# Performance work log

Measured on AMD Instinct MI355X. Metric: run time of the kernel, lower is better.

Reference implementation:

```python
import jax, jax.numpy as jnp
import numpy as np

B, T, D = 2, 2048, 1024
N_HEADS = 16
HEAD_DIM = D // N_HEADS


def setup_inputs() -> dict:
    key = jax.random.key(0)
    ks = jax.random.split(key, 5)
    s = 0.02
    return {
        "x": jax.random.normal(ks[0], (B, T, D), jnp.float32),
        "wq": jax.random.normal(ks[1], (D, D), jnp.float32) * s,
        "wk": jax.random.normal(ks[2], (D, D), jnp.float32) * s,
        "wv": jax.random.normal(ks[3], (D, D), jnp.float32) * s,
        "wo": jax.random.normal(ks[4], (D, D), jnp.float32) * s,
        "bo": jnp.zeros((D,), jnp.float32),
    }


def reference(x, wq, wk, wv, wo, bo):
    b, t, _ = x.shape
    # QKV projections (weights stored [d_in, d_out]); reshape to (b, heads, t, head_dim)
    def split_heads(y):
        return y.reshape(b, t, N_HEADS, HEAD_DIM).transpose(0, 2, 1, 3)
    q = split_heads(x @ wq)
    k = split_heads(x @ wk)
    v = split_heads(x @ wv)
    # causal attention scores: (b, h, t, t)
    scores = jnp.einsum("bhqd,bhkd->bhqk", q, k)
    causal = jnp.tril(jnp.ones((t, t), bool))  # True where attending allowed
    scores = jnp.where(causal, scores, -jnp.inf)
    attn = jax.nn.softmax(scores / np.sqrt(HEAD_DIM).astype(np.float32), axis=-1)
    # dropout_rate = 0.0 (eval mode) -> identity
    ctx = jnp.einsum("bhqk,bhkd->bhqd", attn, v)
    ctx = ctx.transpose(0, 2, 1, 3).reshape(b, t, D)
    return ctx @ wo + bo
```

## Files before the change

kernel.cpp:

```cpp
#include <hip/hip_runtime.h>
#include <hip/hip_bf16.h>
#include <cstdint>

typedef __hip_bfloat16 bf16;
typedef __bf16 bf16x8 __attribute__((ext_vector_type(8)));
typedef __bf16 bf16x4 __attribute__((ext_vector_type(4)));
typedef float f32x4 __attribute__((ext_vector_type(4)));
typedef uint32_t u32x4 __attribute__((ext_vector_type(4)));

#define LOG2E 1.4426950408889634f

__device__ __forceinline__ void gload_lds16(const void* g, void* l) {
  __builtin_amdgcn_global_load_lds(
      (const __attribute__((address_space(1))) unsigned int*)g,
      (__attribute__((address_space(3))) unsigned int*)l,
      16, 0, 0);
}

__device__ __forceinline__ uint32_t pack_bf16(float a, float b) {
  const uint32_t ha = (uint32_t)__builtin_bit_cast(uint16_t, (__bf16)a);
  const uint32_t hb = (uint32_t)__builtin_bit_cast(uint16_t, (__bf16)b);
  return ha | (hb << 16);
}

__global__ void conv_k(const float* __restrict__ src, bf16* __restrict__ dst, int n) {
  const int i = (blockIdx.x * 256 + threadIdx.x) * 8;
  if (i >= n) return;
  const f32x4 a = *(const f32x4*)(src + i);
  const f32x4 b = *(const f32x4*)(src + i + 4);
  bf16x8 o;
#pragma unroll
  for (int j = 0; j < 4; ++j) { o[j] = (__bf16)a[j]; o[4 + j] = (__bf16)b[j]; }
  *(bf16x8*)(dst + i) = o;
}

__global__ void transpose_conv4(
    const float* __restrict__ wq, const float* __restrict__ wk,
    const float* __restrict__ wv, const float* __restrict__ wo,
    bf16* __restrict__ dqkv, bf16* __restrict__ dout) {
  __shared__ float tile[32][33];
  const int z = blockIdx.z;
  const float* src = (z == 0) ? wq : ((z == 1) ? wk : ((z == 2) ? wv : wo));
  bf16* dst = (z < 3) ? (dqkv + (long)z * 1048576) : dout;
  const int bx = blockIdx.x * 32, by = blockIdx.y * 32;
  const int tx = threadIdx.x;
  for (int j = threadIdx.y; j < 32; j += 8)
    tile[j][tx] = src[(long)(by + j) * 1024 + bx + tx];
  __syncthreads();
  for (int j = threadIdx.y; j < 32; j += 8)
    dst[(long)(bx + j) * 1024 + by + tx] = __float2bfloat16(tile[tx][j]);
}

__global__ __launch_bounds__(256, 2) void gemm_qkv(
    const bf16* __restrict__ A, const bf16* __restrict__ Bt,
    bf16* __restrict__ Cq, bf16* __restrict__ Ck, bf16* __restrict__ Cv,
    int M, int N, int K) {
  __shared__ __align__(16) bf16 As[128 * 32];
  __shared__ __align__(16) bf16 Bs[128 * 32];

  const int tid = threadIdx.x;
  const int lane = tid & 63;
  const int wave = tid >> 6;
  const int quad = lane >> 4;
  const int l16 = lane & 15;
  const int m0 = blockIdx.y * 128;
  const int n0 = blockIdx.x * 128;
  const int wm = (wave >> 1) * 64;
  const int wn = (wave & 1) * 64;

  const f32x4 zero4 = {0.f, 0.f, 0.f, 0.f};
  f32x4 acc[4][4];
#pragma unroll
  for (int mi = 0; mi < 4; ++mi)
#pragma unroll
    for (int ni = 0; ni < 4; ++ni) acc[mi][ni] = zero4;

  const int sRow = tid >> 2;
  const int sK = (tid & 3) * 8;
  const bf16* Ag = A + (long)(m0 + sRow) * K + sK;
  const bf16* Ag2 = Ag + 64L * K;
  const bf16* Bg = Bt + (long)(n0 + sRow) * K + sK;
  const bf16* Bg2 = Bg + 64L * K;

  for (int k0 = 0; k0 < K; k0 += 32) {
    gload_lds16(Ag + k0, &As[tid * 8]);
    gload_lds16(Ag2 + k0, &As[tid * 8 + 2048]);
    gload_lds16(Bg + k0, &Bs[tid * 8]);
    gload_lds16(Bg2 + k0, &Bs[tid * 8 + 2048]);
    __syncthreads();

    bf16x8 af[4], bfv[4];
#pragma unroll
    for (int mi = 0; mi < 4; ++mi)
      af[mi] = *(const bf16x8*)&As[(wm + mi * 16 + l16) * 32 + quad * 8];
#pragma unroll
    for (int ni = 0; ni < 4; ++ni)
      bfv[ni] = *(const bf16x8*)&Bs[(wn + ni * 16 + l16) * 32 + quad * 8];
#pragma unroll
    for (int mi = 0; mi < 4; ++mi)
#pragma unroll
      for (int ni = 0; ni < 4; ++ni)
        acc[mi][ni] = __builtin_amdgcn_mfma_f32_16x16x32_bf16(af[mi], bfv[ni], acc[mi][ni], 0, 0, 0);
    __syncthreads();
  }

#pragma unroll
  for (int mi = 0; mi < 4; ++mi) {
    const int gmb = m0 + wm + mi * 16 + quad * 4;
#pragma unroll
    for (int ni = 0; ni < 4; ++ni) {
      const int n = n0 + wn + ni * 16 + l16;
      const int which = n >> 10, rem = n & 1023;
      const int h = rem >> 6, hd = rem & 63;
      bf16* dst = (which == 0) ? Cq : ((which == 1) ? Ck : Cv);
#pragma unroll
      for (int r = 0; r < 4; ++r) {
        const int gm = gmb + r;
        const int b = gm >> 11, t = gm & 2047;
        dst[(((long)(b * 16 + h)) * 2048 + t) * 64 + hd] = __float2bfloat16(acc[mi][ni][r]);
      }
    }
  }
}

__global__ __launch_bounds__(256, 4) void gemm_out(
    const bf16* __restrict__ A, const bf16* __restrict__ Bt,
    const float* __restrict__ bias, float* __restrict__ Cout,
    int M, int N, int K) {
  __shared__ __align__(16) bf16 As[64 * 32];
  __shared__ __align__(16) bf16 Bs[128 * 32];

  const int tid = threadIdx.x;
  const int lane = tid & 63;
  const int wave = tid >> 6;
  const int quad = lane >> 4;
  const int l16 = lane & 15;
  const int m0 = blockIdx.y * 64;
  const int n0 = blockIdx.x * 128;
  const int wm = (wave & 1) * 32;
  const int wn = (wave >> 1) * 64;

  const f32x4 zero4 = {0.f, 0.f, 0.f, 0.f};
  f32x4 acc[2][4];
#pragma unroll
  for (int mi = 0; mi < 2; ++mi)
#pragma unroll
    for (int ni = 0; ni < 4; ++ni) acc[mi][ni] = zero4;

  const int sRow = tid >> 2;
  const int sK = (tid & 3) * 8;
  const bf16* Ag = A + (long)(m0 + sRow) * K + sK;
  const bf16* Bg = Bt + (long)(n0 + sRow) * K + sK;
  const bf16* Bg2 = Bg + 64L * K;

  for (int k0 = 0; k0 < K; k0 += 32) {
    gload_lds16(Ag + k0, &As[tid * 8]);
    gload_lds16(Bg + k0, &Bs[tid * 8]);
    gload_lds16(Bg2 + k0, &Bs[tid * 8 + 2048]);
    __syncthreads();

    bf16x8 af[2], bfv[4];
#pragma unroll
    for (int mi = 0; mi < 2; ++mi)
      af[mi] = *(const bf16x8*)&As[(wm + mi * 16 + l16) * 32 + quad * 8];
#pragma unroll
    for (int ni = 0; ni < 4; ++ni)
      bfv[ni] = *(const bf16x8*)&Bs[(wn + ni * 16 + l16) * 32 + quad * 8];
#pragma unroll
    for (int mi = 0; mi < 2; ++mi)
#pragma unroll
      for (int ni = 0; ni < 4; ++ni)
        acc[mi][ni] = __builtin_amdgcn_mfma_f32_16x16x32_bf16(af[mi], bfv[ni], acc[mi][ni], 0, 0, 0);
    __syncthreads();
  }

#pragma unroll
  for (int mi = 0; mi < 2; ++mi) {
    const int gmb = m0 + wm + mi * 16 + quad * 4;
#pragma unroll
    for (int ni = 0; ni < 4; ++ni) {
      const int n = n0 + wn + ni * 16 + l16;
      const float bv = bias[n];
#pragma unroll
      for (int r = 0; r < 4; ++r)
        Cout[(long)(gmb + r) * N + n] = acc[mi][ni][r] + bv;
    }
  }
}

__global__ __launch_bounds__(256, 3) void attn_kernel(
    const bf16* __restrict__ Q, const bf16* __restrict__ Kg, const bf16* __restrict__ Vg,
    bf16* __restrict__ ctx) {
  constexpr int KSTR = 72, VSTR = 136;
  __shared__ __align__(16) bf16 Ks[128 * KSTR];
  __shared__ __align__(16) bf16 Vt[64 * VSTR];

  const int tid = threadIdx.x;
  const int lane = tid & 63;
  const int wave = tid >> 6;
  const int quad = lane >> 4;
  const int l16 = lane & 15;

  const int id = (int)blockIdx.y * 16 + (int)blockIdx.x;
  const int g = id & 7;
  const int bh = g * 4 + ((id >> 3) & 3);
  const int p = id >> 5;

  const long base = (long)bh * 2048 * 64;
  const int b = bh >> 4, h = bh & 15;

  const int krow = tid >> 1;
  const int kc32 = (tid & 1) * 32;
  const int vr4 = (tid & 31) * 4;
  const int vd8 = (tid >> 5) * 8;
  const int vb4 = (vr4 >> 4) & 1;
  const int vc4 = (vr4 & ~31) + 8 * (((vr4 >> 2) & 3) ^ vb4) + 4 * vb4;

  const float negsh = -12.0f * LOG2E;
  const f32x4 zero4 = {0.f, 0.f, 0.f, 0.f};

#pragma unroll 1
  for (int seg = 0; seg < 2; ++seg) {
    const int qt = seg ? (31 - p) : p;
    const int qbase = qt * 64 + wave * 16;
    const int q = qbase + l16;

    bf16x8 qf0 = *(const bf16x8*)(Q + base + (long)(qbase + l16) * 64 + quad * 8);
    bf16x8 qf1 = *(const bf16x8*)(Q + base + (long)(qbase + l16) * 64 + 32 + quad * 8);
#pragma unroll
    for (int j = 0; j < 8; ++j) {
      qf0[j] = (__bf16)((float)qf0[j] * 0.125f);
      qf1[j] = (__bf16)((float)qf1[j] * 0.125f);
    }

    float l_i = 0.f;
    f32x4 oacc[4];
#pragma unroll
    for (int nb = 0; nb < 4; ++nb) oacc[nb] = zero4;

    const int nk = (qt + 2) >> 1;
    bf16x8 kr[4], vv[4];
    {
      const bf16* kp = Kg + base + (long)krow * 64 + kc32;
#pragma unroll
      for (int i = 0; i < 4; ++i) kr[i] = *(const bf16x8*)(kp + i * 8);
#pragma unroll
      for (int i = 0; i < 4; ++i)
        vv[i] = *(const bf16x8*)(Vg + base + (long)(vr4 + i) * 64 + vd8);
    }

    for (int kt = 0; kt < nk; ++kt) {
      const int k0 = kt * 128;
#pragma unroll
      for (int i = 0; i < 4; ++i)
        *(bf16x8*)&Ks[krow * KSTR + kc32 + i * 8] = kr[i];
#pragma unroll
      for (int j = 0; j < 8; ++j) {
        bf16x4 t;
        t[0] = vv[0][j]; t[1] = vv[1][j]; t[2] = vv[2][j]; t[3] = vv[3][j];
        *(bf16x4*)&Vt[(vd8 + j) * VSTR + vc4] = t;
      }
      __syncthreads();
      if (kt + 1 < nk) {
        const bf16* kp = Kg + base + (long)(k0 + 128 + krow) * 64 + kc32;
#pragma unroll
        for (int i = 0; i < 4; ++i) kr[i] = *(const bf16x8*)(kp + i * 8);
#pragma unroll
        for (int i = 0; i < 4; ++i)
          vv[i] = *(const bf16x8*)(Vg + base + (long)(k0 + 128 + vr4 + i) * 64 + vd8);
      }

      f32x4 s8[8];
      __builtin_amdgcn_s_setprio(1);
#pragma unroll
      for (int kb = 0; kb < 8; ++kb) {
        const bf16x8 kb0 = *(const bf16x8*)&Ks[(kb * 16 + l16) * KSTR + quad * 8];
        const bf16x8 kb1 = *(const bf16x8*)&Ks[(kb * 16 + l16) * KSTR + 32 + quad * 8];
        f32x4 a = zero4;
        a = __builtin_amdgcn_mfma_f32_16x16x32_bf16(kb0, qf0, a, 0, 0, 0);
        a = __builtin_amdgcn_mfma_f32_16x16x32_bf16(kb1, qf1, a, 0, 0, 0);
        s8[kb] = a;
      }
      __builtin_amdgcn_s_setprio(0);

      if (kt == nk - 1) {
        const int qg = q - k0 - quad * 4;
#pragma unroll
        for (int kb = 0; kb < 8; ++kb)
#pragma unroll
          for (int r = 0; r < 4; ++r)
            s8[kb][r] = (kb * 16 + r <= qg) ? s8[kb][r] : -1e30f;
      }

      float rsum = 0.f;
      u32x4 paw[4];
#pragma unroll
      for (int kk = 0; kk < 4; ++kk) {
        const float p0 = exp2f(fmaf(s8[2 * kk][0], LOG2E, negsh));
        const float p1 = exp2f(fmaf(s8[2 * kk][1], LOG2E, negsh));
        const float p2 = exp2f(fmaf(s8[2 * kk][2], LOG2E, negsh));
        const float p3 = exp2f(fmaf(s8[2 * kk][3], LOG2E, negsh));
        const float p4 = exp2f(fmaf(s8[2 * kk + 1][0], LOG2E, negsh));
        const float p5 = exp2f(fmaf(s8[2 * kk + 1][1], LOG2E, negsh));
        const float p6 = exp2f(fmaf(s8[2 * kk + 1][2], LOG2E, negsh));
        const float p7 = exp2f(fmaf(s8[2 * kk + 1][3], LOG2E, negsh));
        rsum += ((p0 + p1) + (p2 + p3)) + ((p4 + p5) + (p6 + p7));
        u32x4 w;
        w[0] = pack_bf16(p0, p1);
        w[1] = pack_bf16(p2, p3);
        w[2] = (uint32_t)__shfl_xor((int)pack_bf16(p4, p5), 16);
        w[3] = (uint32_t)__shfl_xor((int)pack_bf16(p6, p7), 16);
        paw[kk] = w;
      }

      __builtin_amdgcn_s_setprio(1);
#pragma unroll
      for (int kk = 0; kk < 4; ++kk) {
        const bf16x8 pa = __builtin_bit_cast(bf16x8, paw[kk]);
#pragma unroll
        for (int nb2 = 0; nb2 < 4; ++nb2) {
          const bf16x8 vb = *(const bf16x8*)&Vt[(nb2 * 16 + l16) * VSTR + kk * 32 + quad * 8];
          oacc[nb2] = __builtin_amdgcn_mfma_f32_16x16x32_bf16(pa, vb, oacc[nb2], 0, 0, 0);
        }
      }
      __builtin_amdgcn_s_setprio(0);

      rsum += __shfl_xor(rsum, 16);
      rsum += __shfl_xor(rsum, 32);
      l_i += rsum;
      __syncthreads();
    }

    float linv[4];
#pragma unroll
    for (int r = 0; r < 4; ++r) linv[r] = 1.0f / __shfl(l_i, quad * 4 + r);
#pragma unroll
    for (int r = 0; r < 4; ++r) {
      const int t = qbase + quad * 4 + r;
#pragma unroll
      for (int nb2 = 0; nb2 < 4; ++nb2) {
        const int d = h * 64 + nb2 * 16 + l16;
        ctx[((long)b * 2048 + t) * 1024 + d] = __float2bfloat16(oacc[nb2][r] * linv[r]);
      }
    }
  }
}

extern "C" void kernel_launch(void* const* d_in, const int* in_sizes, int n_in,
                              void* d_out, int out_size, void* d_ws, size_t ws_size,
                              hipStream_t stream) {
  const float* x  = (const float*)d_in[0];
  const float* wq = (const float*)d_in[1];
  const float* wk = (const float*)d_in[2];
  const float* wv = (const float*)d_in[3];
  const float* wo = (const float*)d_in[4];
  const float* bo = (const float*)d_in[5];
  float* out = (float*)d_out;

  bf16* Wtqkv = (bf16*)d_ws;
  bf16* Wto   = Wtqkv + 3145728;
  bf16* xb    = Wto + 1048576;
  bf16* Qb    = xb + 4194304;
  bf16* Kb    = Qb + 4194304;
  bf16* Vb    = Kb + 4194304;
  bf16* Cx    = xb;

  hipLaunchKernelGGL(conv_k, dim3(2048), dim3(256), 0, stream, x, xb, 4194304);
  hipLaunchKernelGGL(transpose_conv4, dim3(32, 32, 4), dim3(32, 8), 0, stream,
                     wq, wk, wv, wo, Wtqkv, Wto);

  hipLaunchKernelGGL(gemm_qkv, dim3(24, 32), dim3(256), 0, stream,
                     xb, Wtqkv, Qb, Kb, Vb, 4096, 3072, 1024);

  hipLaunchKernelGGL(attn_kernel, dim3(16, 32), dim3(256), 0, stream, Qb, Kb, Vb, Cx);

  hipLaunchKernelGGL(gemm_out, dim3(8, 64), dim3(256), 0, stream,
                     Cx, Wto, bo, out, 4096, 1024, 1024);
}
```

Before: 185.6 us.

## Double-buffer attention K/V LDS tiles and remap GEMM block indices for XCD locality

The attention kernel now keeps two LDS buffers for K and transposed V. Each next tile is written into the spare buffer after the current tile's MFMAs, which cuts one of the two barriers per iteration. The QKV GEMM remaps block ids so that neighbouring N-tiles land on the same XCD to improve L2 reuse, and the output GEMM's launch bound changes from 4 to 3 blocks per CU with a linearised block index. The doubled LDS footprint in attention may lower occupancy below the requested 3 blocks per CU.

```diff
diff --git a/kernel.cpp b/kernel.cpp
--- a/kernel.cpp
+++ b/kernel.cpp
@@ -63,8 +63,12 @@
   const int wave = tid >> 6;
   const int quad = lane >> 4;
   const int l16 = lane & 15;
-  const int m0 = blockIdx.y * 128;
-  const int n0 = blockIdx.x * 128;
+  const int id = (int)blockIdx.y * 24 + (int)blockIdx.x;
+  const int xcd = id & 7, idx = id >> 3;
+  const int bxn = xcd * 3 + idx % 3;
+  const int byn = idx / 3;
+  const int m0 = byn * 128;
+  const int n0 = bxn * 128;
   const int wm = (wave >> 1) * 64;
   const int wn = (wave & 1) * 64;
 
@@ -123,7 +127,7 @@
   }
 }
 
-__global__ __launch_bounds__(256, 4) void gemm_out(
+__global__ __launch_bounds__(256, 3) void gemm_out(
     const bf16* __restrict__ A, const bf16* __restrict__ Bt,
     const float* __restrict__ bias, float* __restrict__ Cout,
     int M, int N, int K) {
@@ -135,8 +139,9 @@
   const int wave = tid >> 6;
   const int quad = lane >> 4;
   const int l16 = lane & 15;
-  const int m0 = blockIdx.y * 64;
-  const int n0 = blockIdx.x * 128;
+  const int id = (int)blockIdx.y * 8 + (int)blockIdx.x;
+  const int m0 = (id >> 3) * 64;
+  const int n0 = (id & 7) * 128;
   const int wm = (wave & 1) * 32;
   const int wn = (wave >> 1) * 64;
 
@@ -192,8 +197,8 @@
     const bf16* __restrict__ Q, const bf16* __restrict__ Kg, const bf16* __restrict__ Vg,
     bf16* __restrict__ ctx) {
   constexpr int KSTR = 72, VSTR = 136;
-  __shared__ __align__(16) bf16 Ks[128 * KSTR];
-  __shared__ __align__(16) bf16 Vt[64 * VSTR];
+  __shared__ __align__(16) bf16 Ks[2][128 * KSTR];
+  __shared__ __align__(16) bf16 Vt[2][64 * VSTR];
 
   const int tid = threadIdx.x;
   const int lane = tid & 63;
@@ -248,19 +253,24 @@
       for (int i = 0; i < 4; ++i)
         vv[i] = *(const bf16x8*)(Vg + base + (long)(vr4 + i) * 64 + vd8);
     }
-
+    __syncthreads();
+#pragma unroll
+    for (int i = 0; i < 4; ++i)
+      *(bf16x8*)&Ks[0][krow * KSTR + kc32 + i * 8] = kr[i];
+#pragma unroll
+    for (int j = 0; j < 8; ++j) {
+      bf16x4 t;
+      t[0] = vv[0][j]; t[1] = vv[1][j]; t[2] = vv[2][j]; t[3] = vv[3][j];
+      *(bf16x4*)&Vt[0][(vd8 + j) * VSTR + vc4] = t;
+    }
+
+    int cur = 0;
     for (int kt = 0; kt < nk; ++kt) {
+      __syncthreads();
       const int k0 = kt * 128;
-#pragma unroll
-      for (int i = 0; i < 4; ++i)
-        *(bf16x8*)&Ks[krow * KSTR + kc32 + i * 8] = kr[i];
-#pragma unroll
-      for (int j = 0; j < 8; ++j) {
-        bf16x4 t;
-        t[0] = vv[0][j]; t[1] = vv[1][j]; t[2] = vv[2][j]; t[3] = vv[3][j];
-        *(bf16x4*)&Vt[(vd8 + j) * VSTR + vc4] = t;
-      }
-      __syncthreads();
+      const bf16* ksc = &Ks[cur][0];
+      const bf16* vtc = &Vt[cur][0];
+
       if (kt + 1 < nk) {
         const bf16* kp = Kg + base + (long)(k0 + 128 + krow) * 64 + kc32;
 #pragma unroll
@@ -274,8 +284,8 @@
       __builtin_amdgcn_s_setprio(1);
 #pragma unroll
       for (int kb = 0; kb < 8; ++kb) {
-        const bf16x8 kb0 = *(const bf16x8*)&Ks[(kb * 16 + l16) * KSTR + quad * 8];
-        const bf16x8 kb1 = *(const bf16x8*)&Ks[(kb * 16 + l16) * KSTR + 32 + quad * 8];
+        const bf16x8 kb0 = *(const bf16x8*)&ksc[(kb * 16 + l16) * KSTR + quad * 8];
+        const bf16x8 kb1 = *(const bf16x8*)&ksc[(kb * 16 + l16) * KSTR + 32 + quad * 8];
         f32x4 a = zero4;
         a = __builtin_amdgcn_mfma_f32_16x16x32_bf16(kb0, qf0, a, 0, 0, 0);
         a = __builtin_amdgcn_mfma_f32_16x16x32_bf16(kb1, qf1, a, 0, 0, 0);
@@ -319,7 +329,7 @@
         const bf16x8 pa = __builtin_bit_cast(bf16x8, paw[kk]);
 #pragma unroll
         for (int nb2 = 0; nb2 < 4; ++nb2) {
-          const bf16x8 vb = *(const bf16x8*)&Vt[(nb2 * 16 + l16) * VSTR + kk * 32 + quad * 8];
+          const bf16x8 vb = *(const bf16x8*)&vtc[(nb2 * 16 + l16) * VSTR + kk * 32 + quad * 8];
           oacc[nb2] = __builtin_amdgcn_mfma_f32_16x16x32_bf16(pa, vb, oacc[nb2], 0, 0, 0);
         }
       }
@@ -328,7 +338,21 @@
       rsum += __shfl_xor(rsum, 16);
       rsum += __shfl_xor(rsum, 32);
       l_i += rsum;
-      __syncthreads();
+
+      if (kt + 1 < nk) {
+        bf16* ksn = &Ks[cur ^ 1][0];
+        bf16* vtn = &Vt[cur ^ 1][0];
+#pragma unroll
+        for (int i = 0; i < 4; ++i)
+          *(bf16x8*)&ksn[krow * KSTR + kc32 + i * 8] = kr[i];
+#pragma unroll
+        for (int j = 0; j < 8; ++j) {
+          bf16x4 t;
+          t[0] = vv[0][j]; t[1] = vv[1][j]; t[2] = vv[2][j]; t[3] = vv[3][j];
+          *(bf16x4*)&vtn[(vd8 + j) * VSTR + vc4] = t;
+        }
+      }
+      cur ^= 1;
     }
 
     float linv[4];
```

Measured after the change: 185.1 us. Within noise of the previous version (-0.3%).

## Deepen QKV GEMM K-tile to 64 with XOR-swizzled LDS and XCD-aware block remap

Applied to the files above, without the earlier changes.

The QKV projection GEMM now stages 64-wide K slices per barrier instead of 32. The LDS layout uses an XOR swizzle to avoid bank conflicts on the wider rows. Block IDs are remapped so each XCD gets a contiguous group of N tiles, which aims to improve L2 reuse of the weight tiles. The output GEMM gets a trivial id remap and a lower occupancy hint in launch_bounds; doubled LDS per block may reduce occupancy.

```diff
diff --git a/kernel.cpp b/kernel.cpp
--- a/kernel.cpp
+++ b/kernel.cpp
@@ -55,16 +55,20 @@
     const bf16* __restrict__ A, const bf16* __restrict__ Bt,
     bf16* __restrict__ Cq, bf16* __restrict__ Ck, bf16* __restrict__ Cv,
     int M, int N, int K) {
-  __shared__ __align__(16) bf16 As[128 * 32];
-  __shared__ __align__(16) bf16 Bs[128 * 32];
+  __shared__ __align__(16) bf16 As[128 * 64];
+  __shared__ __align__(16) bf16 Bs[128 * 64];
 
   const int tid = threadIdx.x;
   const int lane = tid & 63;
   const int wave = tid >> 6;
   const int quad = lane >> 4;
   const int l16 = lane & 15;
-  const int m0 = blockIdx.y * 128;
-  const int n0 = blockIdx.x * 128;
+  const int id = (int)blockIdx.y * 24 + (int)blockIdx.x;
+  const int xcd = id & 7, idx = id >> 3;
+  const int bxn = xcd * 3 + idx % 3;
+  const int byn = idx / 3;
+  const int m0 = byn * 128;
+  const int n0 = bxn * 128;
   const int wm = (wave >> 1) * 64;
   const int wn = (wave & 1) * 64;
 
@@ -75,32 +79,37 @@
 #pragma unroll
     for (int ni = 0; ni < 4; ++ni) acc[mi][ni] = zero4;
 
-  const int sRow = tid >> 2;
-  const int sK = (tid & 3) * 8;
-  const bf16* Ag = A + (long)(m0 + sRow) * K + sK;
-  const bf16* Ag2 = Ag + 64L * K;
-  const bf16* Bg = Bt + (long)(n0 + sRow) * K + sK;
-  const bf16* Bg2 = Bg + 64L * K;
-
-  for (int k0 = 0; k0 < K; k0 += 32) {
-    gload_lds16(Ag + k0, &As[tid * 8]);
-    gload_lds16(Ag2 + k0, &As[tid * 8 + 2048]);
-    gload_lds16(Bg + k0, &Bs[tid * 8]);
-    gload_lds16(Bg2 + k0, &Bs[tid * 8 + 2048]);
+  const int sRow = tid >> 3;
+  const int sK = (tid & 7) * 8;
+  const int sSwz = sK ^ (8 * (sRow & 7));
+  const bf16* Ag = A + (long)(m0 + sRow) * K + sSwz;
+  const bf16* Bg = Bt + (long)(n0 + sRow) * K + sSwz;
+  const int swzr = 8 * (l16 & 7);
+
+  for (int k0 = 0; k0 < K; k0 += 64) {
+#pragma unroll
+    for (int j = 0; j < 4; ++j) {
+      gload_lds16(Ag + k0 + (long)(32 * j) * K, &As[tid * 8 + 2048 * j]);
+      gload_lds16(Bg + k0 + (long)(32 * j) * K, &Bs[tid * 8 + 2048 * j]);
+    }
     __syncthreads();
 
-    bf16x8 af[4], bfv[4];
-#pragma unroll
-    for (int mi = 0; mi < 4; ++mi)
-      af[mi] = *(const bf16x8*)&As[(wm + mi * 16 + l16) * 32 + quad * 8];
-#pragma unroll
-    for (int ni = 0; ni < 4; ++ni)
-      bfv[ni] = *(const bf16x8*)&Bs[(wn + ni * 16 + l16) * 32 + quad * 8];
-#pragma unroll
-    for (int mi = 0; mi < 4; ++mi)
+#pragma unroll
+    for (int ks = 0; ks < 64; ks += 32) {
+      const int colr = (ks + quad * 8) ^ swzr;
+      bf16x8 af[4], bfv[4];
+#pragma unroll
+      for (int mi = 0; mi < 4; ++mi)
+        af[mi] = *(const bf16x8*)&As[(wm + mi * 16 + l16) * 64 + colr];
 #pragma unroll
       for (int ni = 0; ni < 4; ++ni)
-        acc[mi][ni] = __builtin_amdgcn_mfma_f32_16x16x32_bf16(af[mi], bfv[ni], acc[mi][ni], 0, 0, 0);
+        bfv[ni] = *(const bf16x8*)&Bs[(wn + ni * 16 + l16) * 64 + colr];
+#pragma unroll
+      for (int mi = 0; mi < 4; ++mi)
+#pragma unroll
+        for (int ni = 0; ni < 4; ++ni)
+          acc[mi][ni] = __builtin_amdgcn_mfma_f32_16x16x32_bf16(af[mi], bfv[ni], acc[mi][ni], 0, 0, 0);
+    }
     __syncthreads();
   }
 
@@ -123,7 +132,7 @@
   }
 }
 
-__global__ __launch_bounds__(256, 4) void gemm_out(
+__global__ __launch_bounds__(256, 3) void gemm_out(
     const bf16* __restrict__ A, const bf16* __restrict__ Bt,
     const float* __restrict__ bias, float* __restrict__ Cout,
     int M, int N, int K) {
@@ -135,8 +144,9 @@
   const int wave = tid >> 6;
   const int quad = lane >> 4;
   const int l16 = lane & 15;
-  const int m0 = blockIdx.y * 64;
-  const int n0 = blockIdx.x * 128;
+  const int id = (int)blockIdx.y * 8 + (int)blockIdx.x;
+  const int m0 = (id >> 3) * 64;
+  const int n0 = (id & 7) * 128;
   const int wm = (wave & 1) * 32;
   const int wn = (wave >> 1) * 64;
 
```

After: 182.3 us. No clear change (-1.8%).
